# Kernel optimization log

Hardware: AMD Instinct MI355X
Metric: run time of the kernel (lower is better)

## Reference

```python
import jax, jax.numpy as jnp
import numpy as np

D_MODEL = 1024
D_STATE = 16
D_CONV = 4
EXPAND = 2
D_INNER = EXPAND * D_MODEL          # 2048
DT_RANK = (D_MODEL + 15) // 16      # 64
B_SZ, L = 2, 2048


def setup_inputs() -> dict:
    key = jax.random.key(0)
    ks = jax.random.split(key, 14)
    s = 0.02
    dt_init = jax.random.uniform(ks[10], (D_INNER,), minval=1e-3, maxval=0.1)
    A = jnp.tile(jnp.arange(1, D_STATE + 1, dtype=jnp.float32)[None, :], (D_INNER, 1))
    return {
        "x_f": jax.random.normal(ks[0], (B_SZ, L, D_MODEL), jnp.float32),
        "x_h": jax.random.normal(ks[1], (B_SZ, L, D_MODEL), jnp.float32),
        "W_hf": s * jax.random.normal(ks[2], (D_MODEL, D_MODEL), jnp.float32),
        "b_hf": jnp.zeros((D_MODEL,), jnp.float32),
        "W_in": s * jax.random.normal(ks[3], (2 * D_INNER, D_MODEL), jnp.float32),
        "conv_w": s * jax.random.normal(ks[4], (D_INNER, 1, D_CONV), jnp.float32),
        "conv_b": jnp.zeros((D_INNER,), jnp.float32),
        "W_x": s * jax.random.normal(ks[5], (DT_RANK + 2 * D_STATE, D_INNER), jnp.float32),
        "W_dt": (DT_RANK ** -0.5) * jax.random.normal(ks[6], (D_INNER, DT_RANK), jnp.float32),
        "b_dt": jnp.log(jnp.expm1(dt_init)),
        "A_log": jnp.log(A),
        "D": jnp.ones((D_INNER,), jnp.float32),
        "W_out": s * jax.random.normal(ks[7], (D_MODEL, D_INNER), jnp.float32),
    }


def _mamba(x, W_in, conv_w, conv_b, W_x, W_dt, b_dt, A_log, D, W_out):
    B, Lx, _ = x.shape
    # in_proj -> x, z branches  [B, L, 2*d_inner]
    xz = jnp.einsum("bld,ed->ble", x, W_in)
    x_in, z = jnp.split(xz, 2, axis=-1)
    # causal depthwise conv1d, kernel d_conv, groups = d_inner
    x_nch = jnp.transpose(x_in, (0, 2, 1))  # [B, d_inner, L]
    x_conv = jax.lax.conv_general_dilated(
        x_nch, conv_w, window_strides=(1,), padding=[(D_CONV - 1, 0)],
        dimension_numbers=("NCH", "OIH", "NCH"), feature_group_count=D_INNER)
    x_c = jax.nn.silu(jnp.transpose(x_conv, (0, 2, 1)) + conv_b)  # [B, L, d_inner]
    # input-dependent dt, B, C
    x_dbl = jnp.einsum("ble,fe->blf", x_c, W_x)
    dt_r = x_dbl[..., :DT_RANK]
    B_ssm = x_dbl[..., DT_RANK:DT_RANK + D_STATE]          # [B, L, d_state]
    C_ssm = x_dbl[..., DT_RANK + D_STATE:]                  # [B, L, d_state]
    dt = jax.nn.softplus(jnp.einsum("blr,er->ble", dt_r, W_dt) + b_dt)  # [B, L, d_inner]
    A = -jnp.exp(A_log)  # [d_inner, d_state]

    # selective scan over time; carry h: [B, d_inner, d_state]
    def step(h, inp):
        dt_t, B_t, C_t, x_t = inp  # [B,d_inner], [B,d_state], [B,d_state], [B,d_inner]
        dA = jnp.exp(dt_t[:, :, None] * A)                       # [B, d_inner, d_state]
        dBx = dt_t[:, :, None] * B_t[:, None, :] * x_t[:, :, None]
        h = dA * h + dBx
        y_t = jnp.einsum("bes,bs->be", h, C_t)
        return h, y_t

    seq = (jnp.transpose(dt, (1, 0, 2)), jnp.transpose(B_ssm, (1, 0, 2)),
           jnp.transpose(C_ssm, (1, 0, 2)), jnp.transpose(x_c, (1, 0, 2)))
    h0 = jnp.zeros((B, D_INNER, D_STATE), x.dtype)
    _, ys = jax.lax.scan(step, h0, seq)
    y = jnp.transpose(ys, (1, 0, 2)) + D * x_c   # skip term
    y = y * jax.nn.silu(z)                        # output gate
    return jnp.einsum("ble,de->bld", y, W_out)


def reference(x_f, x_h, W_hf, b_hf, W_in, conv_w, conv_b, W_x, W_dt, b_dt, A_log, D, W_out):
    hf_gate = jax.nn.sigmoid(jnp.einsum("bld,ed->ble", x_h, W_hf) + b_hf)
    modulated = x_f * hf_gate
    return _mamba(modulated, W_in, conv_w, conv_b, W_x, W_dt, b_dt, A_log, D, W_out)
```

## Files before the change

kernel.cpp:

```cpp
#include <hip/hip_runtime.h>
#include <hip/hip_bf16.h>
#include <math.h>

#define L_SEQ  2048
#define BATCH  2
#define DMODEL 1024
#define DINNER 2048
#define DSTATE 16
#define NCHUNK 64
#define LCH    (L_SEQ / NCHUNK)

typedef __attribute__((ext_vector_type(8))) short bf16x8;
typedef __attribute__((ext_vector_type(4))) float f32x4;

__device__ __forceinline__ unsigned short f2bu(float x) {
    __hip_bfloat16 h = __float2bfloat16(x);
    return __builtin_bit_cast(unsigned short, h);
}
__device__ __forceinline__ float bu2f(unsigned short u) {
    __hip_bfloat16 h = __builtin_bit_cast(__hip_bfloat16, u);
    return __bfloat162float(h);
}
__device__ __forceinline__ float fast_exp2(float x) {
    float r; asm("v_exp_f32 %0, %1" : "=v"(r) : "v"(x)); return r;
}
#define LOG2E 1.44269504088896f

__global__ __launch_bounds__(256) void cvt_all(
    const float* __restrict__ Wout, const float* __restrict__ Win,
    const float* __restrict__ xh,   const float* __restrict__ Whf,
    const float* __restrict__ Wx,   const float* __restrict__ Wdt,
    __hip_bfloat16* __restrict__ dWout, __hip_bfloat16* __restrict__ dWin,
    __hip_bfloat16* __restrict__ dxh,   __hip_bfloat16* __restrict__ dWhf,
    __hip_bfloat16* __restrict__ dWx,   __hip_bfloat16* __restrict__ dWdt)
{
    int bid = blockIdx.x;
    const float* s; __hip_bfloat16* d;
    if (bid < 2048)       { s = Wout; d = dWout; }
    else if (bid < 6144)  { s = Win;  d = dWin;  bid -= 2048; }
    else if (bid < 10240) { s = xh;   d = dxh;   bid -= 6144; }
    else if (bid < 11264) { s = Whf;  d = dWhf;  bid -= 10240; }
    else if (bid < 11520) {
        bid -= 11264;
        const int i = (bid * 256 + threadIdx.x) * 4;
        const int r = i >> 11;
        ushort4 u = {0, 0, 0, 0};
        if (r < 96) {
            const float4 v = *reinterpret_cast<const float4*>(&Wx[i]);
            u.x = f2bu(v.x); u.y = f2bu(v.y); u.z = f2bu(v.z); u.w = f2bu(v.w);
        }
        *reinterpret_cast<ushort4*>(&dWx[i]) = u;
        return;
    }
    else                  { s = Wdt;  d = dWdt;  bid -= 11520; }
    const int i = (bid * 256 + threadIdx.x) * 4;
    const float4 v = *reinterpret_cast<const float4*>(&s[i]);
    ushort4 u;
    u.x = f2bu(v.x); u.y = f2bu(v.y); u.z = f2bu(v.z); u.w = f2bu(v.w);
    *reinterpret_cast<ushort4*>(&d[i]) = u;
}

template <int EPI>
__global__ __launch_bounds__(256) void mfma_gemm(
    const __hip_bfloat16* __restrict__ A, int lda,
    const __hip_bfloat16* __restrict__ Bw, int ldb,
    int ksz,
    float* __restrict__ Cf, int ldc,
    __hip_bfloat16* __restrict__ Cb,
    __hip_bfloat16* __restrict__ Cb2,
    const float* __restrict__ bias,
    const float* __restrict__ mul, int ldmul)
{
    __shared__ unsigned short As[128 * 32];
    __shared__ unsigned short Bs[128 * 32];
    const int tid = threadIdx.x;
    const int row0 = blockIdx.y * 128;
    const int col0 = blockIdx.x * 128;
    const int wid = tid >> 6, lane = tid & 63;
    const int wr = wid >> 1, wc = wid & 1;
    const int fr = lane & 15, fq = lane >> 4;
    const int kz0 = blockIdx.z * ksz;

    f32x4 acc[4][4];
#pragma unroll
    for (int i = 0; i < 4; i++)
#pragma unroll
        for (int j = 0; j < 4; j++) acc[i][j] = (f32x4){0.f, 0.f, 0.f, 0.f};

    const int i0 = tid, i1 = tid + 256;
    const size_t ga0 = (size_t)(row0 + (i0 >> 2)) * lda + (i0 & 3) * 8;
    const size_t ga1 = (size_t)(row0 + (i1 >> 2)) * lda + (i1 & 3) * 8;
    const size_t gb0 = (size_t)(col0 + (i0 >> 2)) * ldb + (i0 & 3) * 8;
    const size_t gb1 = (size_t)(col0 + (i1 >> 2)) * ldb + (i1 & 3) * 8;
    const int nk = ksz >> 5;

    for (int kk = 0; kk < nk; kk++) {
        const int koff = kz0 + kk * 32;
#if __has_builtin(__builtin_amdgcn_global_load_lds)
        __syncthreads();
        __builtin_amdgcn_global_load_lds(
            (const __attribute__((address_space(1))) unsigned int*)(A + ga0 + koff),
            (__attribute__((address_space(3))) unsigned int*)&As[i0 * 8], 16, 0, 0);
        __builtin_amdgcn_global_load_lds(
            (const __attribute__((address_space(1))) unsigned int*)(A + ga1 + koff),
            (__attribute__((address_space(3))) unsigned int*)&As[i1 * 8], 16, 0, 0);
        __builtin_amdgcn_global_load_lds(
            (const __attribute__((address_space(1))) unsigned int*)(Bw + gb0 + koff),
            (__attribute__((address_space(3))) unsigned int*)&Bs[i0 * 8], 16, 0, 0);
        __builtin_amdgcn_global_load_lds(
            (const __attribute__((address_space(1))) unsigned int*)(Bw + gb1 + koff),
            (__attribute__((address_space(3))) unsigned int*)&Bs[i1 * 8], 16, 0, 0);
        __syncthreads();
#else
        const uint4 va0 = *reinterpret_cast<const uint4*>(A + ga0 + koff);
        const uint4 va1 = *reinterpret_cast<const uint4*>(A + ga1 + koff);
        const uint4 vb0 = *reinterpret_cast<const uint4*>(Bw + gb0 + koff);
        const uint4 vb1 = *reinterpret_cast<const uint4*>(Bw + gb1 + koff);
        __syncthreads();
        *reinterpret_cast<uint4*>(&As[i0 * 8]) = va0;
        *reinterpret_cast<uint4*>(&As[i1 * 8]) = va1;
        *reinterpret_cast<uint4*>(&Bs[i0 * 8]) = vb0;
        *reinterpret_cast<uint4*>(&Bs[i1 * 8]) = vb1;
        __syncthreads();
#endif
        bf16x8 af[4], bq[4];
#pragma unroll
        for (int rb = 0; rb < 4; rb++)
            af[rb] = *reinterpret_cast<const bf16x8*>(
                &As[(wr * 64 + rb * 16 + fr) * 32 + fq * 8]);
#pragma unroll
        for (int cb = 0; cb < 4; cb++)
            bq[cb] = *reinterpret_cast<const bf16x8*>(
                &Bs[(wc * 64 + cb * 16 + fr) * 32 + fq * 8]);
#pragma unroll
        for (int rb = 0; rb < 4; rb++)
#pragma unroll
            for (int cb = 0; cb < 4; cb++)
                acc[rb][cb] = __builtin_amdgcn_mfma_f32_16x16x32_bf16(
                    af[rb], bq[cb], acc[rb][cb], 0, 0, 0);
    }

    float* Cz = Cf;
    if (EPI == 0)
        Cz = Cf + (size_t)blockIdx.z * (size_t)(gridDim.y * 128) * ldc;
    const int r0 = row0 + wr * 64, c0 = col0 + wc * 64;
#pragma unroll
    for (int rb = 0; rb < 4; rb++)
#pragma unroll
        for (int cb = 0; cb < 4; cb++) {
            const int col = c0 + cb * 16 + fr;
#pragma unroll
            for (int j = 0; j < 4; j++) {
                const int row = r0 + rb * 16 + fq * 4 + j;
                float v = acc[rb][cb][j];
                if (EPI == 0) {
                    Cz[(size_t)row * ldc + col] = v;
                } else if (EPI == 1) {
                    v = 1.f / (1.f + __expf(-(v + bias[col])));
                    v *= mul[(size_t)row * ldmul + col];
                    Cb[(size_t)row * ldc + col] = __float2bfloat16(v);
                } else if (EPI == 2) {
                    if (col0 < 2048) Cb[(size_t)row * 2048 + col] = __float2bfloat16(v);
                    else             Cb2[(size_t)row * 2048 + col - 2048] = __float2bfloat16(v);
                } else {
                    v += bias[col];
                    v = (v > 20.f) ? v : log1pf(__expf(v));
                    Cb[(size_t)row * ldc + col] = __float2bfloat16(v);
                }
            }
        }
}

__global__ __launch_bounds__(256) void reduce_xdbl(
    const float* __restrict__ part, float* __restrict__ xdbl,
    __hip_bfloat16* __restrict__ dtr)
{
    const int i = blockIdx.x * 256 + threadIdx.x;
    float s = 0.f;
#pragma unroll
    for (int j = 0; j < 8; j++) s += part[(size_t)j * 524288 + i];
    xdbl[i] = s;
    const int col = i & 127;
    if (col < 64) dtr[((i >> 7) << 6) + col] = __float2bfloat16(s);
}

__global__ __launch_bounds__(256) void conv_silu_kernel(
    const __hip_bfloat16* __restrict__ xin_b, const float* __restrict__ cw,
    const float* __restrict__ cb, __hip_bfloat16* __restrict__ xcb)
{
    int gid = blockIdx.x * 256 + threadIdx.x;
    int e = gid & (DINNER - 1);
    int row = gid >> 11;
    int t = row & (L_SEQ - 1);
    float s = cb[e];
#pragma unroll
    for (int j = 0; j < 4; j++) {
        int tt = t - 3 + j;
        if (tt >= 0)
            s = fmaf(cw[e * 4 + j],
                     __bfloat162float(xin_b[(size_t)(row - 3 + j) * 2048 + e]), s);
    }
    xcb[(size_t)row * 2048 + e] = __float2bfloat16(s / (1.f + __expf(-s)));
}

__global__ __launch_bounds__(256) void scan_pass_a(
    const __hip_bfloat16* __restrict__ dtb, const __hip_bfloat16* __restrict__ xcb,
    const float* __restrict__ xdbl, const float* __restrict__ A_log,
    __hip_bfloat16* __restrict__ hloc, __hip_bfloat16* __restrict__ Pp)
{
    __shared__ float sB[LCH][16];
    const int tid = threadIdx.x;
    const int e = (blockIdx.x << 8) + tid;
    const int chunk = blockIdx.y;
    const int b = blockIdx.z;
    const int t0 = chunk * LCH;

    if (tid < LCH * 4) {
        const int r = tid >> 2, sl = tid & 3;
        *(float4*)&sB[r][sl * 4] =
            *(const float4*)&xdbl[(size_t)(b * L_SEQ + t0 + r) * 128 + 64 + sl * 4];
    }
    float av[16];
#pragma unroll
    for (int sq = 0; sq < 4; sq++) {
        const float4 al = *(const float4*)&A_log[e * 16 + sq * 4];
#pragma unroll
        for (int j = 0; j < 4; j++)
            av[sq * 4 + j] = -fast_exp2(((const float*)&al)[j] * LOG2E);
    }
    float h[16];
#pragma unroll
    for (int s = 0; s < 16; s++) h[s] = 0.f;
    float sdt = 0.f;
    __syncthreads();

    const size_t rb = (size_t)(b * L_SEQ + t0) * 2048 + e;
    float dtv_n = __bfloat162float(dtb[rb]);
    float xv_n = __bfloat162float(xcb[rb]);
    for (int t = 0; t < LCH; t++) {
        const float dtv = dtv_n, xv = xv_n;
        if (t + 1 < LCH) {
            dtv_n = __bfloat162float(dtb[rb + (size_t)(t + 1) * 2048]);
            xv_n = __bfloat162float(xcb[rb + (size_t)(t + 1) * 2048]);
        }
        sdt += dtv;
        const float dtx = dtv * xv;
        const float dl2 = dtv * LOG2E;
#pragma unroll
        for (int sq = 0; sq < 4; sq++) {
            const float4 B4 = *(const float4*)&sB[t][sq * 4];
#pragma unroll
            for (int j = 0; j < 4; j++) {
                const int s = sq * 4 + j;
                const float Bv = ((const float*)&B4)[j];
                h[s] = fmaf(fast_exp2(dl2 * av[s]), h[s], Bv * dtx);
            }
        }
    }
    const size_t o = (((size_t)chunk * BATCH + b) * 2048 + e) * 16;
#pragma unroll
    for (int sq = 0; sq < 4; sq++) {
        ushort4 uh, up;
        uh.x = f2bu(h[sq * 4]);     uh.y = f2bu(h[sq * 4 + 1]);
        uh.z = f2bu(h[sq * 4 + 2]); uh.w = f2bu(h[sq * 4 + 3]);
        up.x = f2bu(fast_exp2(av[sq * 4] * sdt * LOG2E));
        up.y = f2bu(fast_exp2(av[sq * 4 + 1] * sdt * LOG2E));
        up.z = f2bu(fast_exp2(av[sq * 4 + 2] * sdt * LOG2E));
        up.w = f2bu(fast_exp2(av[sq * 4 + 3] * sdt * LOG2E));
        *(ushort4*)&hloc[o + sq * 4] = uh;
        *(ushort4*)&Pp[o + sq * 4] = up;
    }
}

__global__ __launch_bounds__(256) void scan_pass_b(
    const __hip_bfloat16* __restrict__ hloc, const __hip_bfloat16* __restrict__ Pp,
    __hip_bfloat16* __restrict__ h0)
{
    const int idx = blockIdx.x * 256 + threadIdx.x;
    float h = 0.f;
    h0[idx] = __float2bfloat16(0.f);
    for (int c = 0; c < NCHUNK - 1; c++) {
        const float P = __bfloat162float(Pp[(size_t)c * 65536 + idx]);
        const float hl = __bfloat162float(hloc[(size_t)c * 65536 + idx]);
        h = fmaf(P, h, hl);
        h0[(size_t)(c + 1) * 65536 + idx] = __float2bfloat16(h);
    }
}

__global__ __launch_bounds__(256) void scan_pass_c(
    const __hip_bfloat16* __restrict__ dtb, const __hip_bfloat16* __restrict__ xcb,
    const float* __restrict__ xdbl, const __hip_bfloat16* __restrict__ zb,
    const float* __restrict__ A_log, const float* __restrict__ Dw,
    const __hip_bfloat16* __restrict__ h0, __hip_bfloat16* __restrict__ yb)
{
    __shared__ float sB[LCH][16];
    __shared__ float sC[LCH][16];
    const int tid = threadIdx.x;
    const int e = (blockIdx.x << 8) + tid;
    const int chunk = blockIdx.y;
    const int b = blockIdx.z;
    const int t0 = chunk * LCH;

    if (tid < LCH * 4) {
        const int r = tid >> 2, sl = tid & 3;
        *(float4*)&sB[r][sl * 4] =
            *(const float4*)&xdbl[(size_t)(b * L_SEQ + t0 + r) * 128 + 64 + sl * 4];
    } else if (tid < LCH * 8) {
        const int t2 = tid - LCH * 4;
        const int r = t2 >> 2, sl = t2 & 3;
        *(float4*)&sC[r][sl * 4] =
            *(const float4*)&xdbl[(size_t)(b * L_SEQ + t0 + r) * 128 + 80 + sl * 4];
    }
    float av[16];
#pragma unroll
    for (int sq = 0; sq < 4; sq++) {
        const float4 al = *(const float4*)&A_log[e * 16 + sq * 4];
#pragma unroll
        for (int j = 0; j < 4; j++)
            av[sq * 4 + j] = -fast_exp2(((const float*)&al)[j] * LOG2E);
    }
    const float De = Dw[e];
    float h[16];
    const size_t o = (((size_t)chunk * BATCH + b) * 2048 + e) * 16;
#pragma unroll
    for (int sq = 0; sq < 4; sq++) {
        const ushort4 hv = *(const ushort4*)&h0[o + sq * 4];
        h[sq * 4]     = bu2f(hv.x); h[sq * 4 + 1] = bu2f(hv.y);
        h[sq * 4 + 2] = bu2f(hv.z); h[sq * 4 + 3] = bu2f(hv.w);
    }
    __syncthreads();

    const size_t rb = (size_t)(b * L_SEQ + t0) * 2048 + e;
    float dtv_n = __bfloat162float(dtb[rb]);
    float xv_n = __bfloat162float(xcb[rb]);
    float zv_n = __bfloat162float(zb[rb]);
    for (int t = 0; t < LCH; t++) {
        const float dtv = dtv_n, xv = xv_n, zv = zv_n;
        if (t + 1 < LCH) {
            dtv_n = __bfloat162float(dtb[rb + (size_t)(t + 1) * 2048]);
            xv_n = __bfloat162float(xcb[rb + (size_t)(t + 1) * 2048]);
            zv_n = __bfloat162float(zb[rb + (size_t)(t + 1) * 2048]);
        }
        const float dtx = dtv * xv;
        const float dl2 = dtv * LOG2E;
        float yp0 = 0.f, yp1 = 0.f, yp2 = 0.f, yp3 = 0.f;
#pragma unroll
        for (int sq = 0; sq < 4; sq++) {
            const float4 B4 = *(const float4*)&sB[t][sq * 4];
            const float4 C4 = *(const float4*)&sC[t][sq * 4];
#pragma unroll
            for (int j = 0; j < 4; j++) {
                const int s = sq * 4 + j;
                const float Bv = ((const float*)&B4)[j];
                const float Cv = ((const float*)&C4)[j];
                h[s] = fmaf(fast_exp2(dl2 * av[s]), h[s], Bv * dtx);
                if (sq == 0) yp0 = fmaf(h[s], Cv, yp0);
                else if (sq == 1) yp1 = fmaf(h[s], Cv, yp1);
                else if (sq == 2) yp2 = fmaf(h[s], Cv, yp2);
                else yp3 = fmaf(h[s], Cv, yp3);
            }
        }
        float yv = (yp0 + yp1) + (yp2 + yp3);
        yv = fmaf(De, xv, yv);
        const float sig = 1.f / (1.f + __expf(-zv));
        yb[rb + (size_t)t * 2048] = __float2bfloat16(yv * zv * sig);
    }
}

extern "C" void kernel_launch(void* const* d_in, const int* in_sizes, int n_in,
                              void* d_out, int out_size, void* d_ws, size_t ws_size,
                              hipStream_t stream)
{
    const float* x_f    = (const float*)d_in[0];
    const float* x_h    = (const float*)d_in[1];
    const float* W_hf   = (const float*)d_in[2];
    const float* b_hf   = (const float*)d_in[3];
    const float* W_in   = (const float*)d_in[4];
    const float* conv_w = (const float*)d_in[5];
    const float* conv_b = (const float*)d_in[6];
    const float* W_x    = (const float*)d_in[7];
    const float* W_dt   = (const float*)d_in[8];
    const float* b_dt   = (const float*)d_in[9];
    const float* A_log  = (const float*)d_in[10];
    const float* Dw     = (const float*)d_in[11];
    const float* W_out  = (const float*)d_in[12];
    float* out = (float*)d_out;
    float* ws  = (float*)d_ws;

    __hip_bfloat16* wout_b = (__hip_bfloat16*)(ws);
    __hip_bfloat16* win_b  = (__hip_bfloat16*)(ws + 1048576);
    __hip_bfloat16* xh_b   = (__hip_bfloat16*)(ws + 3145728);
    __hip_bfloat16* whf_b  = (__hip_bfloat16*)(ws + 5242880);
    __hip_bfloat16* m_b    = (__hip_bfloat16*)(ws + 5767168);
    __hip_bfloat16* hloc   = (__hip_bfloat16*)(ws + 1048576);
    __hip_bfloat16* Pp     = (__hip_bfloat16*)(ws + 3145728);
    __hip_bfloat16* h0     = (__hip_bfloat16*)(ws + 5242880);
    __hip_bfloat16* wx_b   = (__hip_bfloat16*)(ws + 7864320);
    __hip_bfloat16* wdt_b  = (__hip_bfloat16*)(ws + 7995392);
    __hip_bfloat16* dtr_b  = (__hip_bfloat16*)(ws + 8060928);
    float*          xdbl   = ws + 10289152;
    __hip_bfloat16* xin_b  = (__hip_bfloat16*)(ws + 10813440);
    __hip_bfloat16* z_b    = (__hip_bfloat16*)(ws + 15007744);
    __hip_bfloat16* xc_b   = (__hip_bfloat16*)(ws + 19202048);
    float*          part   = ws + 23396352;
    __hip_bfloat16* dt_b   = (__hip_bfloat16*)(ws + 27590656);
    __hip_bfloat16* yb     = (__hip_bfloat16*)(ws + 31784960);

    cvt_all<<<11648, 256, 0, stream>>>(
        W_out, W_in, x_h, W_hf, W_x, W_dt,
        wout_b, win_b, xh_b, whf_b, wx_b, wdt_b);

    mfma_gemm<1><<<dim3(8, 32, 1), 256, 0, stream>>>(
        xh_b, DMODEL, whf_b, DMODEL, DMODEL,
        nullptr, DMODEL, m_b, nullptr, b_hf, x_f, DMODEL);

    mfma_gemm<2><<<dim3(32, 32, 1), 256, 0, stream>>>(
        m_b, DMODEL, win_b, DMODEL, DMODEL,
        nullptr, 2048, xin_b, z_b, nullptr, nullptr, 0);

    conv_silu_kernel<<<32768, 256, 0, stream>>>(
        xin_b, conv_w, conv_b, xc_b);

    mfma_gemm<0><<<dim3(1, 32, 8), 256, 0, stream>>>(
        xc_b, DINNER, wx_b, DINNER, 256,
        part, 128, nullptr, nullptr, nullptr, nullptr, 0);
    reduce_xdbl<<<2048, 256, 0, stream>>>(part, xdbl, dtr_b);

    mfma_gemm<3><<<dim3(16, 32, 1), 256, 0, stream>>>(
        dtr_b, 64, wdt_b, 64, 64,
        nullptr, 2048, dt_b, nullptr, b_dt, nullptr, 0);

    scan_pass_a<<<dim3(8, NCHUNK - 1, BATCH), 256, 0, stream>>>(
        dt_b, xc_b, xdbl, A_log, hloc, Pp);
    scan_pass_b<<<256, 256, 0, stream>>>(hloc, Pp, h0);
    scan_pass_c<<<dim3(8, NCHUNK, BATCH), 256, 0, stream>>>(
        dt_b, xc_b, xdbl, z_b, A_log, Dw, h0, yb);

    mfma_gemm<0><<<dim3(8, 32, 1), 256, 0, stream>>>(
        yb, DINNER, wout_b, DINNER, DINNER,
        out, DMODEL, nullptr, nullptr, nullptr, nullptr, 0);
}
```

Baseline: 306.2 us.

## Add dedicated 256x256 double-buffered GEMM for in_proj with direct global-to-LDS loads

Replaces the generic 128x128 templated GEMM for the in_proj x/z split with a specialized kernel. It uses 256x256 tiles, 512 threads and a K-step of 64. LDS is double-buffered and filled with global_load_lds, so the next tile loads while MFMAs run on the current one. The larger tile raises arithmetic intensity and cuts the number of blocks. The cost is about 128KB of LDS per block, which limits occupancy to one block per CU, plus possible LDS bank conflicts from the unswizzled row layout. The unused EPI==2 path and its extra pointer argument are removed from the generic GEMM.

```diff
diff --git a/kernel.cpp b/kernel.cpp
--- a/kernel.cpp
+++ b/kernel.cpp
@@ -60,6 +60,108 @@
     *reinterpret_cast<ushort4*>(&d[i]) = u;
 }
 
+__global__ __launch_bounds__(512) void mfma_gemm256(
+    const __hip_bfloat16* __restrict__ A,
+    const __hip_bfloat16* __restrict__ Bw,
+    __hip_bfloat16* __restrict__ Cb,
+    __hip_bfloat16* __restrict__ Cb2)
+{
+    __shared__ unsigned short As[2][256 * 64];
+    __shared__ unsigned short Bs[2][256 * 64];
+    const int tid = threadIdx.x;
+    const int row0 = blockIdx.y * 256;
+    const int col0 = blockIdx.x * 256;
+    const int wid = tid >> 6, lane = tid & 63;
+    const int wr = wid >> 2, wc = wid & 3;
+    const int fr = lane & 15, fq = lane >> 4;
+
+    f32x4 acc[8][4];
+#pragma unroll
+    for (int m = 0; m < 8; m++)
+#pragma unroll
+        for (int n = 0; n < 4; n++) acc[m][n] = (f32x4){0.f, 0.f, 0.f, 0.f};
+
+    size_t gA[4], gB[4];
+    int ld0[4];
+#pragma unroll
+    for (int l = 0; l < 4; l++) {
+        const int item = l * 512 + tid;
+        const int r = item >> 3, sl = item & 7;
+        gA[l] = (size_t)(row0 + r) * 1024 + sl * 8;
+        gB[l] = (size_t)(col0 + r) * 1024 + sl * 8;
+        ld0[l] = item * 8;
+    }
+
+#if __has_builtin(__builtin_amdgcn_global_load_lds)
+    auto STAGE = [&](int buf, int koff) {
+#pragma unroll
+        for (int l = 0; l < 4; l++)
+            __builtin_amdgcn_global_load_lds(
+                (const __attribute__((address_space(1))) unsigned int*)(A + gA[l] + koff),
+                (__attribute__((address_space(3))) unsigned int*)&As[buf][ld0[l]], 16, 0, 0);
+#pragma unroll
+        for (int l = 0; l < 4; l++)
+            __builtin_amdgcn_global_load_lds(
+                (const __attribute__((address_space(1))) unsigned int*)(Bw + gB[l] + koff),
+                (__attribute__((address_space(3))) unsigned int*)&Bs[buf][ld0[l]], 16, 0, 0);
+    };
+#else
+    auto STAGE = [&](int buf, int koff) {
+#pragma unroll
+        for (int l = 0; l < 4; l++) {
+            *reinterpret_cast<uint4*>(&As[buf][ld0[l]]) =
+                *reinterpret_cast<const uint4*>(A + gA[l] + koff);
+            *reinterpret_cast<uint4*>(&Bs[buf][ld0[l]]) =
+                *reinterpret_cast<const uint4*>(Bw + gB[l] + koff);
+        }
+    };
+#endif
+
+    STAGE(0, 0);
+    __syncthreads();
+    int buf = 0;
+    for (int t = 0; t < 16; t++) {
+        if (t + 1 < 16) STAGE(buf ^ 1, (t + 1) * 64);
+#pragma unroll
+        for (int ks = 0; ks < 2; ks++) {
+            bf16x8 a[8], b[4];
+#pragma unroll
+            for (int m = 0; m < 8; m++)
+                a[m] = *reinterpret_cast<const bf16x8*>(
+                    &As[buf][(wr * 128 + m * 16 + fr) * 64 + ks * 32 + fq * 8]);
+#pragma unroll
+            for (int n = 0; n < 4; n++)
+                b[n] = *reinterpret_cast<const bf16x8*>(
+                    &Bs[buf][(wc * 64 + n * 16 + fr) * 64 + ks * 32 + fq * 8]);
+#pragma unroll
+            for (int m = 0; m < 8; m++)
+#pragma unroll
+                for (int n = 0; n < 4; n++)
+                    acc[m][n] = __builtin_amdgcn_mfma_f32_16x16x32_bf16(
+                        a[m], b[n], acc[m][n], 0, 0, 0);
+        }
+        __syncthreads();
+        buf ^= 1;
+    }
+
+    const int r0 = row0 + wr * 128;
+    const int c0 = col0 + wc * 64;
+    const bool isx = (col0 < 2048);
+#pragma unroll
+    for (int m = 0; m < 8; m++)
+#pragma unroll
+        for (int n = 0; n < 4; n++) {
+            const int col = c0 + n * 16 + fr;
+#pragma unroll
+            for (int j = 0; j < 4; j++) {
+                const int row = r0 + m * 16 + fq * 4 + j;
+                const __hip_bfloat16 v = __float2bfloat16(acc[m][n][j]);
+                if (isx) Cb[(size_t)row * 2048 + col] = v;
+                else     Cb2[(size_t)row * 2048 + col - 2048] = v;
+            }
+        }
+}
+
 template <int EPI>
 __global__ __launch_bounds__(256) void mfma_gemm(
     const __hip_bfloat16* __restrict__ A, int lda,
@@ -67,7 +169,6 @@
     int ksz,
     float* __restrict__ Cf, int ldc,
     __hip_bfloat16* __restrict__ Cb,
-    __hip_bfloat16* __restrict__ Cb2,
     const float* __restrict__ bias,
     const float* __restrict__ mul, int ldmul)
 {
@@ -159,9 +260,6 @@
                     v = 1.f / (1.f + __expf(-(v + bias[col])));
                     v *= mul[(size_t)row * ldmul + col];
                     Cb[(size_t)row * ldc + col] = __float2bfloat16(v);
-                } else if (EPI == 2) {
-                    if (col0 < 2048) Cb[(size_t)row * 2048 + col] = __float2bfloat16(v);
-                    else             Cb2[(size_t)row * 2048 + col - 2048] = __float2bfloat16(v);
                 } else {
                     v += bias[col];
                     v = (v > 20.f) ? v : log1pf(__expf(v));
@@ -412,23 +510,22 @@
 
     mfma_gemm<1><<<dim3(8, 32, 1), 256, 0, stream>>>(
         xh_b, DMODEL, whf_b, DMODEL, DMODEL,
-        nullptr, DMODEL, m_b, nullptr, b_hf, x_f, DMODEL);
-
-    mfma_gemm<2><<<dim3(32, 32, 1), 256, 0, stream>>>(
-        m_b, DMODEL, win_b, DMODEL, DMODEL,
-        nullptr, 2048, xin_b, z_b, nullptr, nullptr, 0);
+        nullptr, DMODEL, m_b, b_hf, x_f, DMODEL);
+
+    mfma_gemm256<<<dim3(16, 16, 1), 512, 0, stream>>>(
+        m_b, win_b, xin_b, z_b);
 
     conv_silu_kernel<<<32768, 256, 0, stream>>>(
         xin_b, conv_w, conv_b, xc_b);
 
     mfma_gemm<0><<<dim3(1, 32, 8), 256, 0, stream>>>(
         xc_b, DINNER, wx_b, DINNER, 256,
-        part, 128, nullptr, nullptr, nullptr, nullptr, 0);
+        part, 128, nullptr, nullptr, nullptr, 0);
     reduce_xdbl<<<2048, 256, 0, stream>>>(part, xdbl, dtr_b);
 
     mfma_gemm<3><<<dim3(16, 32, 1), 256, 0, stream>>>(
         dtr_b, 64, wdt_b, 64, 64,
-        nullptr, 2048, dt_b, nullptr, b_dt, nullptr, 0);
+        nullptr, 2048, dt_b, b_dt, nullptr, 0);
 
     scan_pass_a<<<dim3(8, NCHUNK - 1, BATCH), 256, 0, stream>>>(
         dt_b, xc_b, xdbl, A_log, hloc, Pp);
@@ -438,5 +535,5 @@
 
     mfma_gemm<0><<<dim3(8, 32, 1), 256, 0, stream>>>(
         yb, DINNER, wout_b, DINNER, DINNER,
-        out, DMODEL, nullptr, nullptr, nullptr, nullptr, 0);
-}
+        out, DMODEL, nullptr, nullptr, nullptr, 0);
+}
```

Result: no change. 300.5 us (-1.8%).
